# Optimization experiments

Hardware: AMD Instinct MI355X
Metric: run time of the kernel (lower is better)

## Reference

```python
import jax, jax.numpy as jnp
import numpy as np

B, M, D, S, TOPK = 8, 4096, 512, 128, 64


def setup_inputs() -> dict:
    key = jax.random.key(0)
    ks = jax.random.split(key, 9)
    return {
        "memory": jax.random.normal(ks[0], (B, M, D), jnp.float32),
        "usage": jax.random.uniform(ks[1], (B, M), dtype=jnp.float32),
        "content": jax.random.normal(ks[2], (B, D), jnp.float32),
        "write_strength": jax.random.uniform(ks[3], (B, 1), dtype=jnp.float32),
        "query": jax.random.normal(ks[4], (B, S, D), jnp.float32),
        "key_proj_w": jax.random.normal(ks[5], (D, D), jnp.float32) * 0.02,
        "temporal_table": jax.random.normal(ks[6], (M, D), jnp.float32) * 0.02,
        "usage_decay": jnp.float32(0.99),
        "valid_mask": jax.random.randint(ks[7], (B, M), 0, 2) > 0,
        "write_index": jax.random.randint(ks[8], (B,), 0, M),
        "top_k": TOPK,
    }


def reference(memory, usage, content, write_strength, query, key_proj_w,
              temporal_table, usage_decay, valid_mask, write_index, top_k):
    # ---- write(): soft scatter into the slot selected by write_index ----
    idx = write_index % M                               # [B]
    temporal_emb = temporal_table[idx]                  # [B, D] gather
    content_wt = content + temporal_emb                 # [B, D]
    write_pos = jax.nn.one_hot(idx, M, dtype=memory.dtype)      # [B, M]
    a = write_pos[:, :, None] * write_strength[:, :, None]      # [B, M, 1]
    memory = memory * (1.0 - a) + content_wt[:, None, :] * a    # [B, M, D]
    valid = jnp.logical_or(valid_mask, write_pos > 0)           # [B, M]
    usage = usage * usage_decay + write_pos * write_strength    # [B, M]
    # ---- read(): content-based addressing with top-k masked softmax ----
    keys = jnp.einsum("bmd,ed->bme", memory, key_proj_w)        # Linear, no bias
    scores = jnp.einsum("bsd,bmd->bsm", query, keys) / (D ** 0.5)
    scores = jnp.where(valid[:, None, :], scores, -jnp.inf)
    top_vals = jax.lax.top_k(scores, top_k)[0]                  # [B, S, top_k]
    threshold = top_vals[..., -1:]                              # kth value
    scores = jnp.where(scores < threshold, -jnp.inf, scores)
    attn = jax.nn.softmax(scores, axis=-1)                      # [B, S, M]
    all_invalid = jnp.all(~valid, axis=-1)[:, None, None]
    attn = jnp.where(all_invalid, 0.0, attn)
    retrieved = jnp.einsum("bsm,bmd->bsd", attn, memory)        # [B, S, D]
    return retrieved, attn, usage
```

## Files before the change

### kernel.cpp

```cpp
#include <hip/hip_runtime.h>
#include <hip/hip_bf16.h>
#include <math.h>

#define BB 8
#define MM 4096
#define DD 512
#define SS 128

typedef _Float16 f16;
typedef _Float16 f16x4 __attribute__((ext_vector_type(4)));
typedef _Float16 f16x8 __attribute__((ext_vector_type(8)));
typedef float f32x4 __attribute__((ext_vector_type(4)));

struct f16pair { f16 h; f16 l; };
__device__ __forceinline__ f16pair split2(float x) {
  f16pair p;
  p.h = (f16)x;
  p.l = (f16)(x - (float)p.h);
  return p;
}

__global__ __launch_bounds__(256) void update_kernel(
    float* __restrict__ memory, const float* __restrict__ usage,
    const float* __restrict__ content, const float* __restrict__ wstr,
    const float* __restrict__ ttab, const float* __restrict__ decay_p,
    const int* __restrict__ widx, float* __restrict__ usage_out) {
  const int b = blockIdx.x;
  int idx = widx[b] % MM; if (idx < 0) idx += MM;
  const float ws = wstr[b];
  const float decay = decay_p[0];
  for (int d = threadIdx.x; d < DD; d += blockDim.x) {
    float cw = content[b * DD + d] + ttab[(size_t)idx * DD + d];
    size_t off = (size_t)b * MM * DD + (size_t)idx * DD + d;
    float old = memory[off];
    memory[off] = old * (1.0f - ws) + cw * ws;
  }
  for (int m = threadIdx.x; m < MM; m += blockDim.x) {
    float u = usage[b * MM + m] * decay;
    if (m == idx) u += ws;
    usage_out[b * MM + m] = u;
  }
}

#define QLSTR 40

__global__ __launch_bounds__(256) void gemm_qp_mfma(
    const float* __restrict__ query, const float* __restrict__ W,
    f16* __restrict__ q1, f16* __restrict__ q2) {
  __shared__ __align__(16) f16 A1s[64 * QLSTR];
  __shared__ __align__(16) f16 A2s[64 * QLSTR];
  __shared__ __align__(16) f16 B1s[64 * QLSTR];
  __shared__ __align__(16) f16 B2s[64 * QLSTR];
  const int tid = threadIdx.x;
  const int n0 = blockIdx.x * 64;
  const int r0 = blockIdx.y * 64;
  const int wv = tid >> 6, lane = tid & 63;
  const int quad = lane >> 4, rr = lane & 15;
  const int wr = wv & 1, wc = wv >> 1;

  const int arow = tid >> 3, ak = tid & 7;
  const int bkr = tid >> 4, bnq = tid & 15;

  f32x4 acc[2][2];
#pragma unroll
  for (int i = 0; i < 2; ++i)
#pragma unroll
    for (int j = 0; j < 2; ++j)
#pragma unroll
      for (int c = 0; c < 4; ++c) acc[i][j][c] = 0.f;

  float4 ar0, ar1, br0, br1;
  ar0 = *(const float4*)(query + (size_t)(r0 + arow) * DD + ak * 4);
  ar1 = *(const float4*)(query + (size_t)(r0 + arow + 32) * DD + ak * 4);
  br0 = *(const float4*)(W + (size_t)bkr * DD + n0 + bnq * 4);
  br1 = *(const float4*)(W + (size_t)(bkr + 16) * DD + n0 + bnq * 4);

  for (int ks = 0; ks < 16; ++ks) {
    if (ks) __syncthreads();
    {
      f16x4 h, l;
      f16pair p;
      p = split2(ar0.x); h[0] = p.h; l[0] = p.l;
      p = split2(ar0.y); h[1] = p.h; l[1] = p.l;
      p = split2(ar0.z); h[2] = p.h; l[2] = p.l;
      p = split2(ar0.w); h[3] = p.h; l[3] = p.l;
      *(f16x4*)&A1s[arow * QLSTR + ak * 4] = h;
      *(f16x4*)&A2s[arow * QLSTR + ak * 4] = l;
      p = split2(ar1.x); h[0] = p.h; l[0] = p.l;
      p = split2(ar1.y); h[1] = p.h; l[1] = p.l;
      p = split2(ar1.z); h[2] = p.h; l[2] = p.l;
      p = split2(ar1.w); h[3] = p.h; l[3] = p.l;
      *(f16x4*)&A1s[(arow + 32) * QLSTR + ak * 4] = h;
      *(f16x4*)&A2s[(arow + 32) * QLSTR + ak * 4] = l;
      float wv4[4] = {br0.x, br0.y, br0.z, br0.w};
#pragma unroll
      for (int i = 0; i < 4; ++i) {
        f16pair q = split2(wv4[i]);
        B1s[(bnq * 4 + i) * QLSTR + bkr] = q.h;
        B2s[(bnq * 4 + i) * QLSTR + bkr] = q.l;
      }
      float wv5[4] = {br1.x, br1.y, br1.z, br1.w};
#pragma unroll
      for (int i = 0; i < 4; ++i) {
        f16pair q = split2(wv5[i]);
        B1s[(bnq * 4 + i) * QLSTR + bkr + 16] = q.h;
        B2s[(bnq * 4 + i) * QLSTR + bkr + 16] = q.l;
      }
    }
    __syncthreads();
    if (ks < 15) {
      int k0 = (ks + 1) * 32;
      ar0 = *(const float4*)(query + (size_t)(r0 + arow) * DD + k0 + ak * 4);
      ar1 = *(const float4*)(query + (size_t)(r0 + arow + 32) * DD + k0 + ak * 4);
      br0 = *(const float4*)(W + (size_t)(k0 + bkr) * DD + n0 + bnq * 4);
      br1 = *(const float4*)(W + (size_t)(k0 + bkr + 16) * DD + n0 + bnq * 4);
    }
    f16x8 a1[2], a2[2];
#pragma unroll
    for (int st = 0; st < 2; ++st) {
      int row = wr * 32 + st * 16 + rr;
      a1[st] = *(const f16x8*)&A1s[row * QLSTR + quad * 8];
      a2[st] = *(const f16x8*)&A2s[row * QLSTR + quad * 8];
    }
#pragma unroll
    for (int ct = 0; ct < 2; ++ct) {
      int col = wc * 32 + ct * 16 + rr;
      f16x8 b1 = *(const f16x8*)&B1s[col * QLSTR + quad * 8];
      f16x8 b2 = *(const f16x8*)&B2s[col * QLSTR + quad * 8];
#pragma unroll
      for (int st = 0; st < 2; ++st) {
        acc[st][ct] = __builtin_amdgcn_mfma_f32_16x16x32_f16(a1[st], b2, acc[st][ct], 0, 0, 0);
        acc[st][ct] = __builtin_amdgcn_mfma_f32_16x16x32_f16(a2[st], b1, acc[st][ct], 0, 0, 0);
        acc[st][ct] = __builtin_amdgcn_mfma_f32_16x16x32_f16(a1[st], b1, acc[st][ct], 0, 0, 0);
      }
    }
  }
#pragma unroll
  for (int st = 0; st < 2; ++st)
#pragma unroll
    for (int ct = 0; ct < 2; ++ct)
#pragma unroll
      for (int reg = 0; reg < 4; ++reg) {
        int row = r0 + wr * 32 + st * 16 + quad * 4 + reg;
        int col = n0 + wc * 32 + ct * 16 + rr;
        f16pair p = split2(acc[st][ct][reg]);
        q1[(size_t)row * DD + col] = p.h;
        q2[(size_t)row * DD + col] = p.l;
      }
}

#define LSTR 40

__global__ __launch_bounds__(256, 2) void gemm_scores_mfma(
    const f16* __restrict__ q1_g, const f16* __restrict__ q2_g,
    const float* __restrict__ mem, float* __restrict__ sc_out) {
  __shared__ __align__(16) f16 m1_s[64 * LSTR];
  __shared__ __align__(16) f16 m2_s[64 * LSTR];
  const int tid = threadIdx.x;
  const int b = blockIdx.x & 7;
  const int j0 = (blockIdx.x >> 3) * 64;
  const int wv = tid >> 6, lane = tid & 63;
  const int quad = lane >> 4, rr = lane & 15;

  const f16* q1b = q1_g + (size_t)b * SS * DD;
  const f16* q2b = q2_g + (size_t)b * SS * DD;
  const int mrow = tid >> 3, mk = tid & 7;
  const float* mbase = mem + ((size_t)b * MM + j0) * DD;

  f32x4 acc[2][4];
#pragma unroll
  for (int i = 0; i < 2; ++i)
#pragma unroll
    for (int j = 0; j < 4; ++j)
#pragma unroll
      for (int c = 0; c < 4; ++c) acc[i][j][c] = 0.f;

  float4 mr0, mr1;
  f16x8 a1c[2], a2c[2], a1n[2], a2n[2];

  mr0 = *(const float4*)(mbase + (size_t)mrow * DD + mk * 4);
  mr1 = *(const float4*)(mbase + (size_t)(mrow + 32) * DD + mk * 4);
#pragma unroll
  for (int st = 0; st < 2; ++st) {
    int srow = wv * 32 + st * 16 + rr;
    a1c[st] = *(const f16x8*)(q1b + (size_t)srow * DD + quad * 8);
    a2c[st] = *(const f16x8*)(q2b + (size_t)srow * DD + quad * 8);
  }

  for (int ks = 0; ks < 16; ++ks) {
    if (ks) __syncthreads();
    {
      f16x4 h, l;
      f16pair p;
      p = split2(mr0.x); h[0] = p.h; l[0] = p.l;
      p = split2(mr0.y); h[1] = p.h; l[1] = p.l;
      p = split2(mr0.z); h[2] = p.h; l[2] = p.l;
      p = split2(mr0.w); h[3] = p.h; l[3] = p.l;
      *(f16x4*)&m1_s[mrow * LSTR + mk * 4] = h;
      *(f16x4*)&m2_s[mrow * LSTR + mk * 4] = l;
      p = split2(mr1.x); h[0] = p.h; l[0] = p.l;
      p = split2(mr1.y); h[1] = p.h; l[1] = p.l;
      p = split2(mr1.z); h[2] = p.h; l[2] = p.l;
      p = split2(mr1.w); h[3] = p.h; l[3] = p.l;
      *(f16x4*)&m1_s[(mrow + 32) * LSTR + mk * 4] = h;
      *(f16x4*)&m2_s[(mrow + 32) * LSTR + mk * 4] = l;
    }
    __syncthreads();
    if (ks < 15) {
      int k0 = (ks + 1) * 32;
      mr0 = *(const float4*)(mbase + (size_t)mrow * DD + k0 + mk * 4);
      mr1 = *(const float4*)(mbase + (size_t)(mrow + 32) * DD + k0 + mk * 4);
#pragma unroll
      for (int st = 0; st < 2; ++st) {
        int srow = wv * 32 + st * 16 + rr;
        a1n[st] = *(const f16x8*)(q1b + (size_t)srow * DD + k0 + quad * 8);
        a2n[st] = *(const f16x8*)(q2b + (size_t)srow * DD + k0 + quad * 8);
      }
    }
#pragma unroll
    for (int jt = 0; jt < 4; ++jt) {
      int brow = jt * 16 + rr;
      f16x8 b1 = *(const f16x8*)&m1_s[brow * LSTR + quad * 8];
      f16x8 b2 = *(const f16x8*)&m2_s[brow * LSTR + quad * 8];
#pragma unroll
      for (int st = 0; st < 2; ++st) {
        acc[st][jt] = __builtin_amdgcn_mfma_f32_16x16x32_f16(a1c[st], b2, acc[st][jt], 0, 0, 0);
        acc[st][jt] = __builtin_amdgcn_mfma_f32_16x16x32_f16(a2c[st], b1, acc[st][jt], 0, 0, 0);
        acc[st][jt] = __builtin_amdgcn_mfma_f32_16x16x32_f16(a1c[st], b1, acc[st][jt], 0, 0, 0);
      }
    }
#pragma unroll
    for (int st = 0; st < 2; ++st) {
      a1c[st] = a1n[st];
      a2c[st] = a2n[st];
    }
  }
  const float scl = 0.04419417382415922f;
  float* C = sc_out + (size_t)b * SS * MM;
#pragma unroll
  for (int st = 0; st < 2; ++st)
#pragma unroll
    for (int jt = 0; jt < 4; ++jt)
#pragma unroll
      for (int reg = 0; reg < 4; ++reg) {
        int srow = wv * 32 + st * 16 + quad * 4 + reg;
        int scol = j0 + jt * 16 + rr;
        C[(size_t)srow * MM + scol] = acc[st][jt][reg] * scl;
      }
}

__device__ __forceinline__ unsigned fkey(float f) {
  unsigned u = __float_as_uint(f);
  return (u & 0x80000000u) ? ~u : (u | 0x80000000u);
}
__device__ __forceinline__ float finv(unsigned u) {
  unsigned b = (u & 0x80000000u) ? (u & 0x7fffffffu) : ~u;
  return __uint_as_float(b);
}

__global__ __launch_bounds__(256) void select_kernel(
    const float* __restrict__ scores, const int* __restrict__ vmask,
    const int* __restrict__ widx, const int* __restrict__ topk,
    const float* __restrict__ memory, float* __restrict__ retrieved,
    float* __restrict__ attn) {
  __shared__ float sc[MM];
  __shared__ int kept[MM];
  __shared__ unsigned histw[4 * 256];
  __shared__ float red[256];
  __shared__ unsigned sh_pref;
  __shared__ int sh_k, sh_nkept;
  __shared__ float sh_zinv;

  const int tid = threadIdx.x;
  const int s = blockIdx.x, b = blockIdx.y;
  int wi = widx[b] % MM; if (wi < 0) wi += MM;
  const float4* srow4 = (const float4*)(scores + ((size_t)b * SS + s) * MM);
  const int4* vrow4 = (const int4*)(vmask + (size_t)b * MM);
  unsigned* hw = histw + (tid >> 6) * 256;

  if (tid == 0) { sh_pref = 0u; sh_nkept = 0; sh_k = topk[0]; }
  for (int i = tid; i < 1024; i += 256) histw[i] = 0u;
  __syncthreads();

  float lmax = -INFINITY;
  for (int m4 = tid; m4 < MM / 4; m4 += 256) {
    float4 v = srow4[m4];
    int4 mk = vrow4[m4];
    int mb = m4 * 4;
    if (!(mk.x || mb + 0 == wi)) v.x = -INFINITY;
    if (!(mk.y || mb + 1 == wi)) v.y = -INFINITY;
    if (!(mk.z || mb + 2 == wi)) v.z = -INFINITY;
    if (!(mk.w || mb + 3 == wi)) v.w = -INFINITY;
    ((float4*)sc)[m4] = v;
    lmax = fmaxf(lmax, fmaxf(fmaxf(v.x, v.y), fmaxf(v.z, v.w)));
    atomicAdd(&hw[fkey(v.x) >> 24], 1u);
    atomicAdd(&hw[fkey(v.y) >> 24], 1u);
    atomicAdd(&hw[fkey(v.z) >> 24], 1u);
    atomicAdd(&hw[fkey(v.w) >> 24], 1u);
  }
  red[tid] = lmax;
  __syncthreads();
#pragma unroll
  for (int off = 128; off > 0; off >>= 1) {
    if (tid < off) red[tid] = fmaxf(red[tid], red[tid + off]);
    __syncthreads();
  }
  const float maxv = red[0];

  for (int pass = 0; pass < 4; ++pass) {
    const int shift = 24 - pass * 8;
    if (pass > 0) {
      const unsigned pref = sh_pref;
      const unsigned hmask = 0xFFFFFFFFu << (shift + 8);
      for (int i = tid; i < 1024; i += 256) histw[i] = 0u;
      __syncthreads();
      for (int m = tid; m < MM; m += 256) {
        unsigned u = fkey(sc[m]);
        if ((u & hmask) == pref) atomicAdd(&hw[(u >> shift) & 0xFFu], 1u);
      }
      __syncthreads();
    }
    if (tid < 64) {
      const int l = tid;
      unsigned h0 = histw[l * 4 + 0] + histw[256 + l * 4 + 0] + histw[512 + l * 4 + 0] + histw[768 + l * 4 + 0];
      unsigned h1 = histw[l * 4 + 1] + histw[256 + l * 4 + 1] + histw[512 + l * 4 + 1] + histw[768 + l * 4 + 1];
      unsigned h2 = histw[l * 4 + 2] + histw[256 + l * 4 + 2] + histw[512 + l * 4 + 2] + histw[768 + l * 4 + 2];
      unsigned h3 = histw[l * 4 + 3] + histw[256 + l * 4 + 3] + histw[512 + l * 4 + 3] + histw[768 + l * 4 + 3];
      unsigned lsum = h0 + h1 + h2 + h3;
      unsigned g = lsum;
#pragma unroll
      for (int off = 1; off < 64; off <<= 1) {
        unsigned t = __shfl_down(g, off, 64);
        if (l + off < 64) g += t;
      }
      unsigned above = g - lsum;
      unsigned suf3 = h3 + above;
      unsigned suf2 = h2 + suf3;
      unsigned suf1 = h1 + suf2;
      unsigned suf0 = h0 + suf1;
      const unsigned kk = (unsigned)sh_k;
      const unsigned prefc = sh_pref;
      unsigned ge, geN;
      ge = suf0; geN = suf1;
      if (ge >= kk && geN < kk) { sh_pref = prefc | ((unsigned)(4 * l + 0) << shift); sh_k = (int)(kk - geN); }
      ge = suf1; geN = suf2;
      if (ge >= kk && geN < kk) { sh_pref = prefc | ((unsigned)(4 * l + 1) << shift); sh_k = (int)(kk - geN); }
      ge = suf2; geN = suf3;
      if (ge >= kk && geN < kk) { sh_pref = prefc | ((unsigned)(4 * l + 2) << shift); sh_k = (int)(kk - geN); }
      ge = suf3; geN = above;
      if (ge >= kk && geN < kk) { sh_pref = prefc | ((unsigned)(4 * l + 3) << shift); sh_k = (int)(kk - geN); }
    }
    __syncthreads();
  }
  const float thr = finv(sh_pref);

  float lz = 0.f;
  for (int m4 = tid; m4 < MM / 4; m4 += 256) {
    float4 v = ((float4*)sc)[m4];
    v.x = (v.x >= thr) ? __expf(v.x - maxv) : 0.f;
    v.y = (v.y >= thr) ? __expf(v.y - maxv) : 0.f;
    v.z = (v.z >= thr) ? __expf(v.z - maxv) : 0.f;
    v.w = (v.w >= thr) ? __expf(v.w - maxv) : 0.f;
    ((float4*)sc)[m4] = v;
    lz += v.x + v.y + v.z + v.w;
  }
  red[tid] = lz;
  __syncthreads();
#pragma unroll
  for (int off = 128; off > 0; off >>= 1) {
    if (tid < off) red[tid] += red[tid + off];
    __syncthreads();
  }
  if (tid == 0) sh_zinv = 1.0f / red[0];
  __syncthreads();
  const float zinv = sh_zinv;

  float4* arow4 = (float4*)(attn + ((size_t)b * SS + s) * MM);
  for (int m4 = tid; m4 < MM / 4; m4 += 256) {
    float4 p = ((float4*)sc)[m4];
    float4 o = make_float4(p.x * zinv, p.y * zinv, p.z * zinv, p.w * zinv);
    arow4[m4] = o;
    int mb = m4 * 4;
    if (p.x > 0.f) kept[atomicAdd(&sh_nkept, 1)] = mb + 0;
    if (p.y > 0.f) kept[atomicAdd(&sh_nkept, 1)] = mb + 1;
    if (p.z > 0.f) kept[atomicAdd(&sh_nkept, 1)] = mb + 2;
    if (p.w > 0.f) kept[atomicAdd(&sh_nkept, 1)] = mb + 3;
  }
  __syncthreads();
  const int nk = sh_nkept;

  float a0 = 0.f, a1 = 0.f;
  const float* mb_ = memory + (size_t)b * MM * DD;
  int i = 0;
  for (; i + 4 <= nk; i += 4) {
    int m0 = kept[i], m1 = kept[i + 1], m2 = kept[i + 2], m3 = kept[i + 3];
    float p0 = sc[m0], p1 = sc[m1], p2 = sc[m2], p3 = sc[m3];
    const float* r0 = mb_ + (size_t)m0 * DD;
    const float* r1 = mb_ + (size_t)m1 * DD;
    const float* r2 = mb_ + (size_t)m2 * DD;
    const float* r3 = mb_ + (size_t)m3 * DD;
    float v0a = r0[tid], v0b = r0[tid + 256];
    float v1a = r1[tid], v1b = r1[tid + 256];
    float v2a = r2[tid], v2b = r2[tid + 256];
    float v3a = r3[tid], v3b = r3[tid + 256];
    a0 += p0 * v0a + p1 * v1a + p2 * v2a + p3 * v3a;
    a1 += p0 * v0b + p1 * v1b + p2 * v2b + p3 * v3b;
  }
  for (; i < nk; ++i) {
    int m = kept[i];
    float p = sc[m];
    const float* mr = mb_ + (size_t)m * DD;
    a0 += p * mr[tid];
    a1 += p * mr[tid + 256];
  }
  float* rrow = retrieved + ((size_t)b * SS + s) * DD;
  rrow[tid] = a0 * zinv;
  rrow[tid + 256] = a1 * zinv;
}

extern "C" void kernel_launch(void* const* d_in, const int* in_sizes, int n_in,
                              void* d_out, int out_size, void* d_ws,
                              size_t ws_size, hipStream_t stream) {
  float* memory = (float*)d_in[0];
  const float* usage = (const float*)d_in[1];
  const float* content = (const float*)d_in[2];
  const float* wstr = (const float*)d_in[3];
  const float* query = (const float*)d_in[4];
  const float* W = (const float*)d_in[5];
  const float* ttab = (const float*)d_in[6];
  const float* decay = (const float*)d_in[7];
  const int* vmask = (const int*)d_in[8];
  const int* widx = (const int*)d_in[9];
  const int* topk = (const int*)d_in[10];

  float* out = (float*)d_out;
  float* retrieved = out;
  float* attn = out + (size_t)BB * SS * DD;
  float* usage_out = attn + (size_t)BB * SS * MM;

  const size_t qsz = (size_t)BB * SS * DD;
  float* scores = (float*)d_ws;
  f16* q1;
  f16* q2;
  size_t need = (size_t)BB * SS * MM * 4 + 2 * qsz * 2;
  if (ws_size >= need) {
    q1 = (f16*)(scores + (size_t)BB * SS * MM);
    q2 = q1 + qsz;
  } else {
    q2 = (f16*)(attn + (size_t)BB * SS * MM) - qsz;
    q1 = q2 - qsz;
  }

  update_kernel<<<BB, 256, 0, stream>>>(memory, usage, content, wstr, ttab,
                                        decay, widx, usage_out);
  gemm_qp_mfma<<<dim3(DD / 64, (BB * SS) / 64), 256, 0, stream>>>(query, W, q1,
                                                                  q2);
  gemm_scores_mfma<<<dim3((MM / 64) * BB), 256, 0, stream>>>(q1, q2, memory,
                                                             scores);
  select_kernel<<<dim3(SS, BB), 256, 0, stream>>>(scores, vmask, widx, topk,
                                                  memory, retrieved, attn);
}
```

Measured before the change: 201.9 us.

## Double-buffer LDS in GEMMs, fuse update with query projection, remap select grid

```diff
diff --git a/kernel.cpp b/kernel.cpp
--- a/kernel.cpp
+++ b/kernel.cpp
@@ -20,133 +20,130 @@
   return p;
 }
 
-__global__ __launch_bounds__(256) void update_kernel(
+__device__ __forceinline__ void split_store4(float4 v, f16* p1, f16* p2) {
+  f16x4 h, l;
+  f16pair p;
+  p = split2(v.x); h[0] = p.h; l[0] = p.l;
+  p = split2(v.y); h[1] = p.h; l[1] = p.l;
+  p = split2(v.z); h[2] = p.h; l[2] = p.l;
+  p = split2(v.w); h[3] = p.h; l[3] = p.l;
+  *(f16x4*)p1 = h;
+  *(f16x4*)p2 = l;
+}
+
+__device__ __forceinline__ void cvt8(const float* p, f16x8& h, f16x8& l) {
+  float4 v0 = *(const float4*)p;
+  float4 v1 = *(const float4*)(p + 4);
+  f16pair q;
+  q = split2(v0.x); h[0] = q.h; l[0] = q.l;
+  q = split2(v0.y); h[1] = q.h; l[1] = q.l;
+  q = split2(v0.z); h[2] = q.h; l[2] = q.l;
+  q = split2(v0.w); h[3] = q.h; l[3] = q.l;
+  q = split2(v1.x); h[4] = q.h; l[4] = q.l;
+  q = split2(v1.y); h[5] = q.h; l[5] = q.l;
+  q = split2(v1.z); h[6] = q.h; l[6] = q.l;
+  q = split2(v1.w); h[7] = q.h; l[7] = q.l;
+}
+
+#define QLSTR 40
+
+__global__ __launch_bounds__(256) void prep_kernel(
     float* __restrict__ memory, const float* __restrict__ usage,
     const float* __restrict__ content, const float* __restrict__ wstr,
     const float* __restrict__ ttab, const float* __restrict__ decay_p,
-    const int* __restrict__ widx, float* __restrict__ usage_out) {
-  const int b = blockIdx.x;
-  int idx = widx[b] % MM; if (idx < 0) idx += MM;
-  const float ws = wstr[b];
-  const float decay = decay_p[0];
-  for (int d = threadIdx.x; d < DD; d += blockDim.x) {
-    float cw = content[b * DD + d] + ttab[(size_t)idx * DD + d];
-    size_t off = (size_t)b * MM * DD + (size_t)idx * DD + d;
-    float old = memory[off];
-    memory[off] = old * (1.0f - ws) + cw * ws;
-  }
-  for (int m = threadIdx.x; m < MM; m += blockDim.x) {
-    float u = usage[b * MM + m] * decay;
-    if (m == idx) u += ws;
-    usage_out[b * MM + m] = u;
-  }
-}
-
-#define QLSTR 40
-
-__global__ __launch_bounds__(256) void gemm_qp_mfma(
+    const int* __restrict__ widx, float* __restrict__ usage_out,
     const float* __restrict__ query, const float* __restrict__ W,
     f16* __restrict__ q1, f16* __restrict__ q2) {
-  __shared__ __align__(16) f16 A1s[64 * QLSTR];
-  __shared__ __align__(16) f16 A2s[64 * QLSTR];
-  __shared__ __align__(16) f16 B1s[64 * QLSTR];
-  __shared__ __align__(16) f16 B2s[64 * QLSTR];
+  __shared__ __align__(16) f16 B1s[2][32 * QLSTR];
+  __shared__ __align__(16) f16 B2s[2][32 * QLSTR];
   const int tid = threadIdx.x;
-  const int n0 = blockIdx.x * 64;
-  const int r0 = blockIdx.y * 64;
+
+  if (blockIdx.x < 8) {
+    const int b = blockIdx.x;
+    int idx = widx[b] % MM; if (idx < 0) idx += MM;
+    const float ws = wstr[b];
+    const float decay = decay_p[0];
+    for (int d = tid; d < DD; d += blockDim.x) {
+      float cw = content[b * DD + d] + ttab[(size_t)idx * DD + d];
+      size_t off = (size_t)b * MM * DD + (size_t)idx * DD + d;
+      float old = memory[off];
+      memory[off] = old * (1.0f - ws) + cw * ws;
+    }
+    for (int m = tid; m < MM; m += blockDim.x) {
+      float u = usage[b * MM + m] * decay;
+      if (m == idx) u += ws;
+      usage_out[b * MM + m] = u;
+    }
+    return;
+  }
+
+  const int bid = blockIdx.x - 8;
+  const int n0 = (bid & 15) * 32;
+  const int r0 = (bid >> 4) * 64;
   const int wv = tid >> 6, lane = tid & 63;
   const int quad = lane >> 4, rr = lane & 15;
   const int wr = wv & 1, wc = wv >> 1;
 
-  const int arow = tid >> 3, ak = tid & 7;
-  const int bkr = tid >> 4, bnq = tid & 15;
-
-  f32x4 acc[2][2];
-#pragma unroll
-  for (int i = 0; i < 2; ++i)
-#pragma unroll
-    for (int j = 0; j < 2; ++j)
-#pragma unroll
-      for (int c = 0; c < 4; ++c) acc[i][j][c] = 0.f;
-
-  float4 ar0, ar1, br0, br1;
-  ar0 = *(const float4*)(query + (size_t)(r0 + arow) * DD + ak * 4);
-  ar1 = *(const float4*)(query + (size_t)(r0 + arow + 32) * DD + ak * 4);
-  br0 = *(const float4*)(W + (size_t)bkr * DD + n0 + bnq * 4);
-  br1 = *(const float4*)(W + (size_t)(bkr + 16) * DD + n0 + bnq * 4);
+  const int krow = tid >> 3, nc = tid & 7;
+
+  f32x4 acc[2];
+#pragma unroll
+  for (int st = 0; st < 2; ++st)
+#pragma unroll
+    for (int c = 0; c < 4; ++c) acc[st][c] = 0.f;
+
+  float4 wv4 = *(const float4*)(W + (size_t)krow * DD + n0 + nc * 4);
+  {
+    float e[4] = {wv4.x, wv4.y, wv4.z, wv4.w};
+#pragma unroll
+    for (int i = 0; i < 4; ++i) {
+      f16pair p = split2(e[i]);
+      B1s[0][(nc * 4 + i) * QLSTR + krow] = p.h;
+      B2s[0][(nc * 4 + i) * QLSTR + krow] = p.l;
+    }
+  }
+  __syncthreads();
 
   for (int ks = 0; ks < 16; ++ks) {
-    if (ks) __syncthreads();
-    {
-      f16x4 h, l;
-      f16pair p;
-      p = split2(ar0.x); h[0] = p.h; l[0] = p.l;
-      p = split2(ar0.y); h[1] = p.h; l[1] = p.l;
-      p = split2(ar0.z); h[2] = p.h; l[2] = p.l;
-      p = split2(ar0.w); h[3] = p.h; l[3] = p.l;
-      *(f16x4*)&A1s[arow * QLSTR + ak * 4] = h;
-      *(f16x4*)&A2s[arow * QLSTR + ak * 4] = l;
-      p = split2(ar1.x); h[0] = p.h; l[0] = p.l;
-      p = split2(ar1.y); h[1] = p.h; l[1] = p.l;
-      p = split2(ar1.z); h[2] = p.h; l[2] = p.l;
-      p = split2(ar1.w); h[3] = p.h; l[3] = p.l;
-      *(f16x4*)&A1s[(arow + 32) * QLSTR + ak * 4] = h;
-      *(f16x4*)&A2s[(arow + 32) * QLSTR + ak * 4] = l;
-      float wv4[4] = {br0.x, br0.y, br0.z, br0.w};
+    const int cur = ks & 1;
+    if (ks < 15)
+      wv4 = *(const float4*)(W + (size_t)((ks + 1) * 32 + krow) * DD + n0 + nc * 4);
+    f16x8 a1[2], a2[2];
+#pragma unroll
+    for (int st = 0; st < 2; ++st) {
+      int arow = r0 + wr * 32 + st * 16 + rr;
+      cvt8(query + (size_t)arow * DD + ks * 32 + quad * 8, a1[st], a2[st]);
+    }
+    int col = wc * 16 + rr;
+    f16x8 b1 = *(const f16x8*)&B1s[cur][col * QLSTR + quad * 8];
+    f16x8 b2 = *(const f16x8*)&B2s[cur][col * QLSTR + quad * 8];
+#pragma unroll
+    for (int st = 0; st < 2; ++st) {
+      acc[st] = __builtin_amdgcn_mfma_f32_16x16x32_f16(a1[st], b2, acc[st], 0, 0, 0);
+      acc[st] = __builtin_amdgcn_mfma_f32_16x16x32_f16(a2[st], b1, acc[st], 0, 0, 0);
+      acc[st] = __builtin_amdgcn_mfma_f32_16x16x32_f16(a1[st], b1, acc[st], 0, 0, 0);
+    }
+    if (ks < 15) {
+      float e[4] = {wv4.x, wv4.y, wv4.z, wv4.w};
 #pragma unroll
       for (int i = 0; i < 4; ++i) {
-        f16pair q = split2(wv4[i]);
-        B1s[(bnq * 4 + i) * QLSTR + bkr] = q.h;
-        B2s[(bnq * 4 + i) * QLSTR + bkr] = q.l;
-      }
-      float wv5[4] = {br1.x, br1.y, br1.z, br1.w};
-#pragma unroll
-      for (int i = 0; i < 4; ++i) {
-        f16pair q = split2(wv5[i]);
-        B1s[(bnq * 4 + i) * QLSTR + bkr + 16] = q.h;
-        B2s[(bnq * 4 + i) * QLSTR + bkr + 16] = q.l;
+        f16pair p = split2(e[i]);
+        B1s[cur ^ 1][(nc * 4 + i) * QLSTR + krow] = p.h;
+        B2s[cur ^ 1][(nc * 4 + i) * QLSTR + krow] = p.l;
       }
     }
     __syncthreads();
-    if (ks < 15) {
-      int k0 = (ks + 1) * 32;
-      ar0 = *(const float4*)(query + (size_t)(r0 + arow) * DD + k0 + ak * 4);
-      ar1 = *(const float4*)(query + (size_t)(r0 + arow + 32) * DD + k0 + ak * 4);
-      br0 = *(const float4*)(W + (size_t)(k0 + bkr) * DD + n0 + bnq * 4);
-      br1 = *(const float4*)(W + (size_t)(k0 + bkr + 16) * DD + n0 + bnq * 4);
-    }
-    f16x8 a1[2], a2[2];
-#pragma unroll
-    for (int st = 0; st < 2; ++st) {
-      int row = wr * 32 + st * 16 + rr;
-      a1[st] = *(const f16x8*)&A1s[row * QLSTR + quad * 8];
-      a2[st] = *(const f16x8*)&A2s[row * QLSTR + quad * 8];
-    }
-#pragma unroll
-    for (int ct = 0; ct < 2; ++ct) {
-      int col = wc * 32 + ct * 16 + rr;
-      f16x8 b1 = *(const f16x8*)&B1s[col * QLSTR + quad * 8];
-      f16x8 b2 = *(const f16x8*)&B2s[col * QLSTR + quad * 8];
-#pragma unroll
-      for (int st = 0; st < 2; ++st) {
-        acc[st][ct] = __builtin_amdgcn_mfma_f32_16x16x32_f16(a1[st], b2, acc[st][ct], 0, 0, 0);
-        acc[st][ct] = __builtin_amdgcn_mfma_f32_16x16x32_f16(a2[st], b1, acc[st][ct], 0, 0, 0);
-        acc[st][ct] = __builtin_amdgcn_mfma_f32_16x16x32_f16(a1[st], b1, acc[st][ct], 0, 0, 0);
-      }
-    }
   }
 #pragma unroll
   for (int st = 0; st < 2; ++st)
 #pragma unroll
-    for (int ct = 0; ct < 2; ++ct)
-#pragma unroll
-      for (int reg = 0; reg < 4; ++reg) {
-        int row = r0 + wr * 32 + st * 16 + quad * 4 + reg;
-        int col = n0 + wc * 32 + ct * 16 + rr;
-        f16pair p = split2(acc[st][ct][reg]);
-        q1[(size_t)row * DD + col] = p.h;
-        q2[(size_t)row * DD + col] = p.l;
-      }
+    for (int reg = 0; reg < 4; ++reg) {
+      int row = r0 + wr * 32 + st * 16 + quad * 4 + reg;
+      int col = n0 + wc * 16 + rr;
+      f16pair p = split2(acc[st][reg]);
+      q1[(size_t)row * DD + col] = p.h;
+      q2[(size_t)row * DD + col] = p.l;
+    }
 }
 
 #define LSTR 40
@@ -154,8 +151,8 @@
 __global__ __launch_bounds__(256, 2) void gemm_scores_mfma(
     const f16* __restrict__ q1_g, const f16* __restrict__ q2_g,
     const float* __restrict__ mem, float* __restrict__ sc_out) {
-  __shared__ __align__(16) f16 m1_s[64 * LSTR];
-  __shared__ __align__(16) f16 m2_s[64 * LSTR];
+  __shared__ __align__(16) f16 m1_s[2][64 * LSTR];
+  __shared__ __align__(16) f16 m2_s[2][64 * LSTR];
   const int tid = threadIdx.x;
   const int b = blockIdx.x & 7;
   const int j0 = (blockIdx.x >> 3) * 64;
@@ -186,26 +183,12 @@
     a1c[st] = *(const f16x8*)(q1b + (size_t)srow * DD + quad * 8);
     a2c[st] = *(const f16x8*)(q2b + (size_t)srow * DD + quad * 8);
   }
+  split_store4(mr0, &m1_s[0][mrow * LSTR + mk * 4], &m2_s[0][mrow * LSTR + mk * 4]);
+  split_store4(mr1, &m1_s[0][(mrow + 32) * LSTR + mk * 4], &m2_s[0][(mrow + 32) * LSTR + mk * 4]);
+  __syncthreads();
 
   for (int ks = 0; ks < 16; ++ks) {
-    if (ks) __syncthreads();
-    {
-      f16x4 h, l;
-      f16pair p;
-      p = split2(mr0.x); h[0] = p.h; l[0] = p.l;
-      p = split2(mr0.y); h[1] = p.h; l[1] = p.l;
-      p = split2(mr0.z); h[2] = p.h; l[2] = p.l;
-      p = split2(mr0.w); h[3] = p.h; l[3] = p.l;
-      *(f16x4*)&m1_s[mrow * LSTR + mk * 4] = h;
-      *(f16x4*)&m2_s[mrow * LSTR + mk * 4] = l;
-      p = split2(mr1.x); h[0] = p.h; l[0] = p.l;
-      p = split2(mr1.y); h[1] = p.h; l[1] = p.l;
-      p = split2(mr1.z); h[2] = p.h; l[2] = p.l;
-      p = split2(mr1.w); h[3] = p.h; l[3] = p.l;
-      *(f16x4*)&m1_s[(mrow + 32) * LSTR + mk * 4] = h;
-      *(f16x4*)&m2_s[(mrow + 32) * LSTR + mk * 4] = l;
-    }
-    __syncthreads();
+    const int cur = ks & 1;
     if (ks < 15) {
       int k0 = (ks + 1) * 32;
       mr0 = *(const float4*)(mbase + (size_t)mrow * DD + k0 + mk * 4);
@@ -220,8 +203,8 @@
 #pragma unroll
     for (int jt = 0; jt < 4; ++jt) {
       int brow = jt * 16 + rr;
-      f16x8 b1 = *(const f16x8*)&m1_s[brow * LSTR + quad * 8];
-      f16x8 b2 = *(const f16x8*)&m2_s[brow * LSTR + quad * 8];
+      f16x8 b1 = *(const f16x8*)&m1_s[cur][brow * LSTR + quad * 8];
+      f16x8 b2 = *(const f16x8*)&m2_s[cur][brow * LSTR + quad * 8];
 #pragma unroll
       for (int st = 0; st < 2; ++st) {
         acc[st][jt] = __builtin_amdgcn_mfma_f32_16x16x32_f16(a1c[st], b2, acc[st][jt], 0, 0, 0);
@@ -229,11 +212,14 @@
         acc[st][jt] = __builtin_amdgcn_mfma_f32_16x16x32_f16(a1c[st], b1, acc[st][jt], 0, 0, 0);
       }
     }
-#pragma unroll
-    for (int st = 0; st < 2; ++st) {
-      a1c[st] = a1n[st];
-      a2c[st] = a2n[st];
-    }
+    if (ks < 15) {
+      const int nxt = cur ^ 1;
+      split_store4(mr0, &m1_s[nxt][mrow * LSTR + mk * 4], &m2_s[nxt][mrow * LSTR + mk * 4]);
+      split_store4(mr1, &m1_s[nxt][(mrow + 32) * LSTR + mk * 4], &m2_s[nxt][(mrow + 32) * LSTR + mk * 4]);
+#pragma unroll
+      for (int st = 0; st < 2; ++st) { a1c[st] = a1n[st]; a2c[st] = a2n[st]; }
+    }
+    __syncthreads();
   }
   const float scl = 0.04419417382415922f;
   float* C = sc_out + (size_t)b * SS * MM;
@@ -272,7 +258,7 @@
   __shared__ float sh_zinv;
 
   const int tid = threadIdx.x;
-  const int s = blockIdx.x, b = blockIdx.y;
+  const int b = blockIdx.x & 7, s = blockIdx.x >> 3;
   int wi = widx[b] % MM; if (wi < 0) wi += MM;
   const float4* srow4 = (const float4*)(scores + ((size_t)b * SS + s) * MM);
   const int4* vrow4 = (const int4*)(vmask + (size_t)b * MM);
@@ -451,12 +437,11 @@
     q1 = q2 - qsz;
   }
 
-  update_kernel<<<BB, 256, 0, stream>>>(memory, usage, content, wstr, ttab,
-                                        decay, widx, usage_out);
-  gemm_qp_mfma<<<dim3(DD / 64, (BB * SS) / 64), 256, 0, stream>>>(query, W, q1,
-                                                                  q2);
+  prep_kernel<<<8 + 256, 256, 0, stream>>>(memory, usage, content, wstr, ttab,
+                                           decay, widx, usage_out, query, W,
+                                           q1, q2);
   gemm_scores_mfma<<<dim3((MM / 64) * BB), 256, 0, stream>>>(q1, q2, memory,
                                                              scores);
-  select_kernel<<<dim3(SS, BB), 256, 0, stream>>>(scores, vmask, widx, topk,
-                                                  memory, retrieved, attn);
-}
+  select_kernel<<<dim3(SS * BB), 256, 0, stream>>>(scores, vmask, widx, topk,
+                                                   memory, retrieved, attn);
+}
```

New measurement: 180.8 us. -10.5%, faster.
